# Optimization experiments

Measured on AMD Instinct MI355X. Metric: run time of the kernel, lower is better.

The kernel has to match this reference:

```python
import jax, jax.numpy as jnp
import numpy as np

# Static configuration (matches init_kwargs)
EMBED_DIM = 256
NUM_HEADS = 8
NUM_LEVELS = 4
NUM_POINTS = 16
N_DEGREE = 3
HEAD_DIM = EMBED_DIM // NUM_HEADS
SPATIAL_SHAPES = ((64, 64), (32, 32), (16, 16), (8, 8))  # (H, W) per level
LEN_V = sum(h * w for h, w in SPATIAL_SHAPES)


def _bilinear_gather(v, loc, Hl, Wl):
    """Bilinear sampling with zero padding, align_corners=False.
    v:   [bs, nH, Hl*Wl, hd]  flattened level feature map (per head)
    loc: [bs, nH, Q, 2]       (x, y) in [0, 1]
    returns [bs, nH, Q, hd]
    """
    x = loc[..., 0] * Wl - 0.5
    y = loc[..., 1] * Hl - 0.5
    x0 = jnp.floor(x)
    y0 = jnp.floor(y)
    wx = x - x0
    wy = y - y0
    out = jnp.zeros(v.shape[:2] + (loc.shape[2], v.shape[-1]), v.dtype)
    corners = ((0, 0, (1 - wx) * (1 - wy)), (1, 0, wx * (1 - wy)),
               (0, 1, (1 - wx) * wy), (1, 1, wx * wy))
    for dx, dy, w in corners:
        xi = x0 + dx
        yi = y0 + dy
        valid = (xi >= 0) & (xi < Wl) & (yi >= 0) & (yi < Hl)
        idx = (jnp.clip(yi, 0, Hl - 1) * Wl + jnp.clip(xi, 0, Wl - 1)).astype(jnp.int32)
        g = jnp.take_along_axis(v, idx[..., None], axis=2)  # [bs,nH,Q,hd]
        out = out + g * (w * valid.astype(w.dtype))[..., None]
    return out


def setup_inputs() -> dict:
    key = jax.random.key(0)
    ks = jax.random.split(key, 12)
    bs, Lq = 4, 1024
    s = 0.02
    return {
        "query": jax.random.normal(ks[0], (bs, Lq, EMBED_DIM), jnp.float32),
        # polynomial coefficients for x(l), y(l); scaled so curves stay roughly in [0,1]
        "reference_points": jax.random.uniform(ks[1], (bs, Lq, 2 * (N_DEGREE + 1)), jnp.float32) * 0.25,
        "value": jax.random.normal(ks[2], (bs, LEN_V, EMBED_DIM), jnp.float32),
        "W_value": jax.random.normal(ks[3], (EMBED_DIM, EMBED_DIM), jnp.float32) * s,
        "b_value": jnp.zeros((EMBED_DIM,), jnp.float32),
        "W_offsets": jax.random.normal(ks[4], (EMBED_DIM, NUM_HEADS * NUM_LEVELS * NUM_POINTS * 2), jnp.float32) * s,
        "b_offsets": jax.random.normal(ks[5], (NUM_HEADS * NUM_LEVELS * NUM_POINTS * 2,), jnp.float32) * 0.5,
        "W_attn": jax.random.normal(ks[6], (EMBED_DIM, NUM_HEADS * NUM_LEVELS * NUM_POINTS), jnp.float32) * s,
        "b_attn": jnp.zeros((NUM_HEADS * NUM_LEVELS * NUM_POINTS,), jnp.float32),
        "W_out": jax.random.normal(ks[7], (EMBED_DIM, EMBED_DIM), jnp.float32) * s,
        "b_out": jnp.zeros((EMBED_DIM,), jnp.float32),
    }


def reference(query, reference_points, value, W_value, b_value, W_offsets,
              b_offsets, W_attn, b_attn, W_out, b_out):
    bs, Lq, _ = query.shape
    Lv = value.shape[1]
    nH, nL, nP, hd = NUM_HEADS, NUM_LEVELS, NUM_POINTS, HEAD_DIM

    v = (value @ W_value + b_value).reshape(bs, Lv, nH, hd)

    sampling_offsets = (query @ W_offsets + b_offsets).reshape(bs, Lq, nH, nL, nP, 2)
    attn = jax.nn.softmax((query @ W_attn + b_attn).reshape(bs, Lq, nH, nL * nP), axis=-1)
    attn = attn.reshape(bs, Lq, nH, nL, nP)

    # reference_points last dim == 8: polynomial branch
    lambdaz = jnp.linspace(0.0, 1.0, nP)
    lambdas = jnp.stack([lambdaz ** i for i in range(N_DEGREE, -1, -1)], axis=1)  # [nP, deg+1]
    ref_polys = reference_points.reshape(bs, Lq, 2, N_DEGREE + 1)
    pnts = jnp.einsum('bqcd,pd->bqpc', ref_polys, lambdas)  # [bs,Lq,nP,2] (x,y)

    # offset_normalizer: spatial shapes flipped -> (W, H) per level
    normalizer = jnp.array([[w, h] for (h, w) in SPATIAL_SHAPES], jnp.float32)
    normalizer = normalizer.reshape(1, 1, 1, nL, 1, 2)
    sampling_locations = pnts[:, :, None, None, :, :] + sampling_offsets / normalizer
    # -> [bs, Lq, nH, nL, nP, 2] in [0,1]

    # deformable attention core: per-level bilinear gather + softmax-weighted sum
    out = jnp.zeros((bs, Lq, nH, hd), v.dtype)
    start = 0
    for lvl, (Hl, Wl) in enumerate(SPATIAL_SHAPES):
        v_l = v[:, start:start + Hl * Wl].transpose(0, 2, 1, 3)  # [bs,nH,Hl*Wl,hd]
        loc_l = sampling_locations[:, :, :, lvl]                 # [bs,Lq,nH,nP,2]
        loc_l = loc_l.transpose(0, 2, 1, 3, 4).reshape(bs, nH, Lq * nP, 2)
        sampled = _bilinear_gather(v_l, loc_l, Hl, Wl).reshape(bs, nH, Lq, nP, hd)
        out = out + jnp.einsum('bhqpd,bqhp->bqhd', sampled, attn[:, :, :, lvl])
        start += Hl * Wl

    output = out.reshape(bs, Lq, nH * hd) @ W_out + b_out
    return output, sampling_locations, attn
```

## Files before the change

kernel.cpp:

```cpp
#include <hip/hip_runtime.h>
#include <math.h>

#define BS 4
#define LQ 1024
#define EMB 256
#define NH 8
#define NL 4
#define NP 16
#define HD 32
#define LV 5440
#define LVP 5936
#define KDIM 256

typedef __attribute__((ext_vector_type(8))) short short8;
typedef __attribute__((ext_vector_type(4))) float f32x4;

__device__ inline unsigned short f2bf(float f) {
    unsigned u = __builtin_bit_cast(unsigned, f);
    u += 0x7fff + ((u >> 16) & 1);
    return (unsigned short)(u >> 16);
}



__global__ __launch_bounds__(256) void prep(const float* __restrict__ Wv,
                                            const float* __restrict__ Wo,
                                            const float* __restrict__ Wa,
                                            const float* __restrict__ Wu,
                                            const float* __restrict__ value,
                                            const float* __restrict__ query,
                                            unsigned short* __restrict__ Wt,
                                            unsigned short* __restrict__ val_bf,
                                            unsigned short* __restrict__ qry_bf,
                                            unsigned short* __restrict__ v_pad) {
    const int blk = blockIdx.x;
    const int t = threadIdx.x;
    if (blk < 512) {
        __shared__ float tile[32][33];
        const int n0 = (blk & 63) * 32, k0 = (blk >> 6) * 32;
        const float* src; int N, nloc;
        if (n0 < 256)       { src = Wv; N = 256;  nloc = n0; }
        else if (n0 < 1280) { src = Wo; N = 1024; nloc = n0 - 256; }
        else if (n0 < 1792) { src = Wa; N = 512;  nloc = n0 - 1280; }
        else                { src = Wu; N = 256;  nloc = n0 - 1792; }
        const int tx = t & 31, ty = t >> 5;
#pragma unroll
        for (int i = 0; i < 32; i += 8)
            tile[ty + i][tx] = src[(size_t)(k0 + ty + i) * N + nloc + tx];
        __syncthreads();
        if (t < 128) {
            const int n_loc = t & 31, oct = t >> 5;
            const int n = n0 + n_loc;
            short8 h;
#pragma unroll
            for (int e = 0; e < 8; ++e) h[e] = (short)f2bf(tile[oct * 8 + e][n_loc]);
            const size_t off = ((size_t)(n >> 4) * 8 + (k0 >> 5)) * 512
                             + ((n & 15) + 16 * oct) * 8;
            *(short8*)(Wt + off) = h;
        }
    } else if (blk < 3744) {
        int i; const float* src; unsigned short* dst;
        if (blk < 3232) { i = (blk - 512) * 256 + t;  src = value; dst = val_bf; }
        else            { i = (blk - 3232) * 256 + t; src = query; dst = qry_bf; }
        const int r = i >> 5, oct = i & 31, k0 = oct * 8;
        const float4 f0 = *(const float4*)(src + (size_t)r * KDIM + k0);
        const float4 f1 = *(const float4*)(src + (size_t)r * KDIM + k0 + 4);
        short8 h;
        h[0] = (short)f2bf(f0.x); h[1] = (short)f2bf(f0.y);
        h[2] = (short)f2bf(f0.z); h[3] = (short)f2bf(f0.w);
        h[4] = (short)f2bf(f1.x); h[5] = (short)f2bf(f1.y);
        h[6] = (short)f2bf(f1.z); h[7] = (short)f2bf(f1.w);
        const size_t off = ((size_t)(r >> 4) * 8 + (oct >> 2)) * 512
                         + ((r & 15) + 16 * (oct & 3)) * 8;
        *(short8*)(dst + off) = h;
    } else {
        const int pidx = (blk - 3744) * 8 + (t >> 5);
        const int lane32 = t & 31;
        const unsigned b = (unsigned)pidx / 496u;
        const unsigned rem = (unsigned)pidx - b * 496u;
        int Wd, W2, pb, i;
        if (rem < 260)      { Wd = 64; W2 = 66; pb = 0;    i = rem; }
        else if (rem < 392) { Wd = 32; W2 = 34; pb = 4356; i = rem - 260; }
        else if (rem < 460) { Wd = 16; W2 = 18; pb = 5512; i = rem - 392; }
        else                { Wd = 8;  W2 = 10; pb = 5836; i = rem - 460; }
        int y, x;
        if (i < W2)          { y = 0;      x = i; }
        else if (i < 2 * W2) { y = Wd + 1; x = i - W2; }
        else { const int j = i - 2 * W2; y = 1 + (j >> 1); x = (j & 1) ? (Wd + 1) : 0; }
        const int hh = lane32 >> 2, cq = lane32 & 3;
        const size_t off = (((size_t)(hh * BS + b) * LVP + pb + y * W2 + x) << 5)
                         + cq * 8;
        uint4 z = {0, 0, 0, 0};
        *(uint4*)(v_pad + off) = z;
    }
}

template <int MODE>
__device__ __forceinline__ void gemm_nolds(const unsigned short* __restrict__ A,
                                           const unsigned short* __restrict__ Bt,
                                           const float* __restrict__ bias,
                                           const float* __restrict__ bias2,
                                           const float* __restrict__ refp,
                                           void* __restrict__ Cv,
                                           float* __restrict__ C2,
                                           int N, int bx, int by) {
    const int t = threadIdx.x;
    const int lane = t & 63, w = t >> 6;
    const int quad = lane >> 4, l16 = lane & 15;
    const int wr = w >> 1, wc = w & 1;
    const int row0 = by * 128, col0 = bx * 128;

    const unsigned short* ap = A  + ((size_t)((row0 >> 4) + wr * 4) * 8) * 512 + lane * 8;
    const unsigned short* bp = Bt + ((size_t)((col0 >> 4) + wc * 4) * 8) * 512 + lane * 8;

    f32x4 acc[4][4] = {};

#pragma unroll 2
    for (int kt = 0; kt < 8; ++kt) {
        short8 af[4], bf[4];
#pragma unroll
        for (int mi = 0; mi < 4; ++mi)
            af[mi] = *(const short8*)(ap + (size_t)mi * 4096 + kt * 512);
#pragma unroll
        for (int ni = 0; ni < 4; ++ni)
            bf[ni] = *(const short8*)(bp + (size_t)ni * 4096 + kt * 512);
#pragma unroll
        for (int mi = 0; mi < 4; ++mi)
#pragma unroll
            for (int ni = 0; ni < 4; ++ni)
                acc[mi][ni] = __builtin_amdgcn_mfma_f32_16x16x32_bf16(af[mi], bf[ni],
                                                                      acc[mi][ni], 0, 0, 0);
    }

    if (MODE == 0) {
#pragma unroll
        for (int ni = 0; ni < 4; ++ni) {
            const int c = col0 + wc * 64 + ni * 16 + l16;
            const float bv = bias[c];
#pragma unroll
            for (int mi = 0; mi < 4; ++mi) {
                const int r0 = row0 + wr * 64 + mi * 16 + quad * 4;
#pragma unroll
                for (int rr = 0; rr < 4; ++rr)
                    ((float*)Cv)[(size_t)(r0 + rr) * N + c] = acc[mi][ni][rr] + bv;
            }
        }
    } else if (MODE == 2) {
        unsigned short* C = (unsigned short*)Cv;
        float bv[4];
        int cc[4];
#pragma unroll
        for (int ni = 0; ni < 4; ++ni) {
            cc[ni] = col0 + wc * 64 + ni * 16 + l16;
            bv[ni] = bias[cc[ni]];
        }
#pragma unroll
        for (int mi = 0; mi < 4; ++mi) {
#pragma unroll
            for (int rr = 0; rr < 4; ++rr) {
                const unsigned r = row0 + wr * 64 + mi * 16 + quad * 4 + rr;
                const unsigned b = r / 5440u;
                const unsigned flat = r - b * 5440u;
                unsigned y, x, W2, pb;
                if (flat < 4096)      { y = flat >> 6; x = flat & 63; W2 = 66; pb = 0; }
                else if (flat < 5120) { const unsigned f = flat - 4096; y = f >> 5; x = f & 31; W2 = 34; pb = 4356; }
                else if (flat < 5376) { const unsigned f = flat - 5120; y = f >> 4; x = f & 15; W2 = 18; pb = 5512; }
                else                  { const unsigned f = flat - 5376; y = f >> 3; x = f & 7;  W2 = 10; pb = 5836; }
                const size_t pix = (size_t)(pb + (y + 1) * W2 + (x + 1)) << 5;
#pragma unroll
                for (int ni = 0; ni < 4; ++ni) {
                    const int cc_ = cc[ni];
                    const size_t off = (((size_t)((cc_ >> 5) * BS + b) * LVP) << 5)
                                     + pix + (cc_ & 31);
                    C[off] = f2bf(acc[mi][ni][rr] + bv[ni]);
                }
            }
        }
    } else {
        const bool is_off = (col0 < 1024);
        if (is_off) {
            float* C = (float*)Cv;
#pragma unroll
            for (int ni = 0; ni < 4; ++ni) {
                const int cg = col0 + wc * 64 + ni * 16 + l16;
                const int xy = cg & 1, p = (cg >> 1) & 15, l = (cg >> 5) & 3;
                const float lam = (float)p * (1.0f / 15.0f);
                const float l2 = lam * lam, l3 = l2 * lam;
                const float rW = (l == 0) ? 0.015625f : (l == 1) ? 0.03125f
                                : (l == 2) ? 0.0625f : 0.125f;
                const float bv = bias[cg];
#pragma unroll
                for (int mi = 0; mi < 4; ++mi) {
                    const int r0 = row0 + wr * 64 + mi * 16 + quad * 4;
#pragma unroll
                    for (int rr = 0; rr < 4; ++rr) {
                        const int r = r0 + rr;
                        const float4 rp = *(const float4*)(refp + (size_t)r * 8 + xy * 4);
                        const float poly = rp.x * l3 + rp.y * l2 + rp.z * lam + rp.w;
                        C[(size_t)r * 1024 + cg] = poly + (acc[mi][ni][rr] + bv) * rW;
                    }
                }
            }
        } else {
            const int cabase = col0 - 1024 + wc * 64;
            float bv[4];
#pragma unroll
            for (int ni = 0; ni < 4; ++ni) bv[ni] = bias2[cabase + ni * 16 + l16];
#pragma unroll
            for (int mi = 0; mi < 4; ++mi) {
                const int r0 = row0 + wr * 64 + mi * 16 + quad * 4;
#pragma unroll
                for (int rr = 0; rr < 4; ++rr) {
                    float v0 = acc[mi][0][rr] + bv[0];
                    float v1 = acc[mi][1][rr] + bv[1];
                    float v2 = acc[mi][2][rr] + bv[2];
                    float v3 = acc[mi][3][rr] + bv[3];
                    float mx = fmaxf(fmaxf(v0, v1), fmaxf(v2, v3));
#pragma unroll
                    for (int mk = 1; mk < 16; mk <<= 1) mx = fmaxf(mx, __shfl_xor(mx, mk));
                    v0 = __expf(v0 - mx); v1 = __expf(v1 - mx);
                    v2 = __expf(v2 - mx); v3 = __expf(v3 - mx);
                    float s = v0 + v1 + v2 + v3;
#pragma unroll
                    for (int mk = 1; mk < 16; mk <<= 1) s += __shfl_xor(s, mk);
                    const float inv = 1.0f / s;
                    const size_t rb = (size_t)(r0 + rr) * 512 + cabase + l16;
                    C2[rb]      = v0 * inv;
                    C2[rb + 16] = v1 * inv;
                    C2[rb + 32] = v2 * inv;
                    C2[rb + 48] = v3 * inv;
                }
            }
        }
    }
}

__global__ __launch_bounds__(256, 3) void gemm_fused(const unsigned short* __restrict__ val_bf,
                                                     const unsigned short* __restrict__ qry_bf,
                                                     const unsigned short* __restrict__ Wt,
                                                     const float* __restrict__ b_value,
                                                     const float* __restrict__ b_off,
                                                     const float* __restrict__ b_attn,
                                                     const float* __restrict__ refp,
                                                     unsigned short* __restrict__ v_pad,
                                                     float* __restrict__ loc_out,
                                                     float* __restrict__ attn_out) {
    const int b = blockIdx.x;
    if (b < 340) {
        gemm_nolds<2>(val_bf, Wt, b_value, nullptr, nullptr,
                      v_pad, nullptr, 256, b & 1, b >> 1);
    } else {
        const int b2 = b - 340;
        gemm_nolds<1>(qry_bf, Wt + (size_t)256 * KDIM, b_off, b_attn, refp,
                      loc_out, attn_out, 1536, b2 % 12, b2 / 12);
    }
}

__global__ __launch_bounds__(256, 8) void gemm_outp64(const unsigned short* __restrict__ interm,
                                                      const unsigned short* __restrict__ Wt_out,
                                                      const float* __restrict__ b_out,
                                                      float* __restrict__ out) {
    const int t = threadIdx.x;
    const int lane = t & 63, w = t >> 6;
    const int quad = lane >> 4, l16 = lane & 15;
    const int wr = w >> 1, wc = w & 1;
    const int bx = blockIdx.x & 3, by = blockIdx.x >> 2;
    const int row0 = by * 64 + wr * 32, col0 = bx * 64 + wc * 32;

    const unsigned short* ap = interm + ((size_t)(row0 >> 4) * 8) * 512 + lane * 8;
    const unsigned short* bp = Wt_out + ((size_t)(col0 >> 4) * 8) * 512 + lane * 8;

    f32x4 acc[2][2] = {};

#pragma unroll 2
    for (int kt = 0; kt < 8; ++kt) {
        short8 af[2], bf[2];
#pragma unroll
        for (int mi = 0; mi < 2; ++mi)
            af[mi] = *(const short8*)(ap + (size_t)mi * 4096 + kt * 512);
#pragma unroll
        for (int ni = 0; ni < 2; ++ni)
            bf[ni] = *(const short8*)(bp + (size_t)ni * 4096 + kt * 512);
#pragma unroll
        for (int mi = 0; mi < 2; ++mi)
#pragma unroll
            for (int ni = 0; ni < 2; ++ni)
                acc[mi][ni] = __builtin_amdgcn_mfma_f32_16x16x32_bf16(af[mi], bf[ni],
                                                                      acc[mi][ni], 0, 0, 0);
    }

#pragma unroll
    for (int ni = 0; ni < 2; ++ni) {
        const int c = col0 + ni * 16 + l16;
        const float bv = b_out[c];
#pragma unroll
        for (int mi = 0; mi < 2; ++mi) {
            const int r0 = row0 + mi * 16 + quad * 4;
#pragma unroll
            for (int rr = 0; rr < 4; ++rr)
                out[(size_t)(r0 + rr) * 256 + c] = acc[mi][ni][rr] + bv;
        }
    }
}

__global__ __launch_bounds__(256, 8) void sample_kernel(const unsigned short* __restrict__ v,
                                                        const float* __restrict__ loc,
                                                        const float* __restrict__ attn,
                                                        unsigned short* __restrict__ interm) {
    const int t = threadIdx.x;
    const int h = blockIdx.x & 7;
    const int bq0 = (blockIdx.x >> 3) * 16;

    __shared__ float4 wls[1088];
    __shared__ unsigned short pls[1088];

    {
        const int gloc = t >> 4;
        const int lvl  = (t >> 2) & 3;
        const int pq   = t & 3;
        const int g = (bq0 + gloc) * 8 + h;
        const float4 l01 = *(const float4*)(loc + (size_t)g * 128 + lvl * 32 + pq * 8);
        const float4 l23 = *(const float4*)(loc + (size_t)g * 128 + lvl * 32 + pq * 8 + 4);
        const float4 av  = *(const float4*)(attn + (size_t)g * 64 + lvl * 16 + pq * 4);
        const int Wd = 64 >> lvl;
        const float Wf = (float)Wd;
        const int W2 = Wd + 2;
        const int pb = (lvl == 0) ? 0 : (lvl == 1) ? 4356 : (lvl == 2) ? 5512 : 5836;
        const int ibase = gloc * 64 + lvl * 16 + pq * 4;
        const int pbase = ibase + (ibase >> 4);
        const float lx[4] = {l01.x, l01.z, l23.x, l23.z};
        const float ly[4] = {l01.y, l01.w, l23.y, l23.w};
        const float aw[4] = {av.x, av.y, av.z, av.w};
#pragma unroll
        for (int k = 0; k < 4; ++k) {
            const float x = fmaf(lx[k], Wf, -0.5f);
            const float y = fmaf(ly[k], Wf, -0.5f);
            const float xc = fminf(fmaxf(x, -1.0f), Wf);
            const float yc = fminf(fmaxf(y, -1.0f), Wf);
            const float x0f = fminf(floorf(xc), Wf - 1.0f);
            const float y0f = fminf(floorf(yc), Wf - 1.0f);
            const float wx = xc - x0f, wy = yc - y0f;
            const float iwx = 1.0f - wx, iwy = 1.0f - wy;
            const int px = (int)x0f + 1;
            const int py = (int)y0f + 1;
            const float a = aw[k];
            wls[pbase + k] = make_float4(iwx * iwy * a, wx * iwy * a,
                                         iwx * wy * a,  wx * wy * a);
            pls[pbase + k] = (unsigned short)(pb + py * W2 + px);
        }
    }
    __syncthreads();

    const int bq = bq0 + (t >> 4);
    const int l16i = t & 15;
    const int lvl = l16i >> 2;
    const int cq  = l16i & 3;
    const int b = bq >> 10;
    const int rowoff = ((64 >> lvl) + 2) * 32;

    const unsigned short* vl = v + (((size_t)(h * BS + b) * LVP) << 5) + cq * 8;
    const int wbase = (t >> 4) * 64 + lvl * 16;
    const int wphys = wbase + (wbase >> 4);

    float2 acc2[4] = {};

    auto cvt2 = [](unsigned d) {
        uint2 u; u.x = d << 16; u.y = d & 0xffff0000u;
        return __builtin_bit_cast(float2, u);
    };
    auto cadd = [&](const uint4 q, float wgt) {
        const float2 w2 = make_float2(wgt, wgt);
        acc2[0] += cvt2(q.x) * w2;
        acc2[1] += cvt2(q.y) * w2;
        acc2[2] += cvt2(q.z) * w2;
        acc2[3] += cvt2(q.w) * w2;
    };

#pragma unroll 1
    for (int p = 0; p < 16; ++p) {
        const float4 w = wls[wphys + p];
        const int base = ((int)pls[wphys + p]) << 5;
        const unsigned short* ptr = vl + base;
        const uint4 g00 = *(const uint4*)(ptr);
        const uint4 g10 = *(const uint4*)(ptr + 32);
        const uint4 g01 = *(const uint4*)(ptr + rowoff);
        const uint4 g11 = *(const uint4*)(ptr + rowoff + 32);
        cadd(g00, w.x); cadd(g10, w.y); cadd(g01, w.z); cadd(g11, w.w);
    }

    float a[8] = {acc2[0].x, acc2[0].y, acc2[1].x, acc2[1].y,
                  acc2[2].x, acc2[2].y, acc2[3].x, acc2[3].y};
#pragma unroll
    for (int m = 4; m <= 8; m <<= 1)
#pragma unroll
        for (int k = 0; k < 8; ++k) a[k] += __shfl_xor(a[k], m);

    if (lvl == 0) {
        unsigned short o[8];
#pragma unroll
        for (int k = 0; k < 8; ++k) o[k] = f2bf(a[k]);
        const size_t off = ((size_t)(bq >> 4) * 8 + h) * 512
                         + ((bq & 15) + 16 * cq) * 8;
        *(uint4*)(interm + off) = *(const uint4*)o;
    }
}

extern "C" void kernel_launch(void* const* d_in, const int* in_sizes, int n_in,
                              void* d_out, int out_size, void* d_ws, size_t ws_size,
                              hipStream_t stream) {
    const float* query   = (const float*)d_in[0];
    const float* refp    = (const float*)d_in[1];
    const float* value   = (const float*)d_in[2];
    const float* W_value = (const float*)d_in[3];
    const float* b_value = (const float*)d_in[4];
    const float* W_off   = (const float*)d_in[5];
    const float* b_off   = (const float*)d_in[6];
    const float* W_attn  = (const float*)d_in[7];
    const float* b_attn  = (const float*)d_in[8];
    const float* W_out   = (const float*)d_in[9];
    const float* b_out   = (const float*)d_in[10];

    float* out      = (float*)d_out;
    float* loc_out  = out + 1048576;
    float* attn_out = out + 5242880;

    char* ws = (char*)d_ws;
    unsigned short* v_pad  = (unsigned short*)ws;
    unsigned short* val_bf = (unsigned short*)(ws + 12156928);
    unsigned short* interm = (unsigned short*)(ws + 12156928);
    unsigned short* qry_bf = (unsigned short*)(ws + 23298048);
    unsigned short* Wt_all = (unsigned short*)(ws + 25395200);

    const dim3 blk(256);

    prep<<<3992, blk, 0, stream>>>(W_value, W_off, W_attn, W_out, value, query,
                                   Wt_all, val_bf, qry_bf, v_pad);

    gemm_fused<<<724, blk, 0, stream>>>(val_bf, qry_bf, Wt_all, b_value, b_off,
                                        b_attn, refp, v_pad, loc_out, attn_out);

    sample_kernel<<<(BS * LQ * NH) / 16, blk, 0, stream>>>(v_pad, loc_out, attn_out, interm);

    gemm_outp64<<<256, blk, 0, stream>>>(interm, Wt_all + (size_t)1792 * KDIM, b_out, out);
}
```

Baseline: 149.6 us.

## Fuse projection GEMMs, sampling and output GEMM into one persistent kernel

Replaces the three launches after prep with one persistent kernel of 720 blocks. It loops over the former GEMM, sampling and output-GEMM work items and separates the phases with atomic-counter grid barriers; prep resets the barrier counters. The aim is to remove kernel launch gaps and tail idle time between stages. In exchange, sampling now runs at most about 3 blocks per CU instead of up to 8. The design also depends on all 720 blocks being resident at once, otherwise the spin barriers could deadlock.

```diff
diff --git a/kernel.cpp b/kernel.cpp
--- a/kernel.cpp
+++ b/kernel.cpp
@@ -12,6 +12,8 @@
 #define LVP 5936
 #define KDIM 256
 
+#define TAIL_GRID 720
+
 typedef __attribute__((ext_vector_type(8))) short short8;
 typedef __attribute__((ext_vector_type(4))) float f32x4;
 
@@ -22,6 +24,17 @@
 }
 
 
+__device__ __forceinline__ void gridbar(unsigned* cnt, unsigned n) {
+    __threadfence();
+    __syncthreads();
+    if (threadIdx.x == 0) {
+        __hip_atomic_fetch_add(cnt, 1u, __ATOMIC_ACQ_REL, __HIP_MEMORY_SCOPE_AGENT);
+        while (__hip_atomic_load(cnt, __ATOMIC_RELAXED, __HIP_MEMORY_SCOPE_AGENT) < n)
+            __builtin_amdgcn_s_sleep(16);
+    }
+    __syncthreads();
+    __threadfence();
+}
 
 __global__ __launch_bounds__(256) void prep(const float* __restrict__ Wv,
                                             const float* __restrict__ Wo,
@@ -32,9 +45,11 @@
                                             unsigned short* __restrict__ Wt,
                                             unsigned short* __restrict__ val_bf,
                                             unsigned short* __restrict__ qry_bf,
-                                            unsigned short* __restrict__ v_pad) {
+                                            unsigned short* __restrict__ v_pad,
+                                            unsigned* __restrict__ bar) {
     const int blk = blockIdx.x;
     const int t = threadIdx.x;
+    if (blk == 0 && t == 0) { bar[0] = 0u; bar[1] = 0u; }
     if (blk < 512) {
         __shared__ float tile[32][33];
         const int n0 = (blk & 63) * 32, k0 = (blk >> 6) * 32;
@@ -235,81 +250,13 @@
     }
 }
 
-__global__ __launch_bounds__(256, 3) void gemm_fused(const unsigned short* __restrict__ val_bf,
-                                                     const unsigned short* __restrict__ qry_bf,
-                                                     const unsigned short* __restrict__ Wt,
-                                                     const float* __restrict__ b_value,
-                                                     const float* __restrict__ b_off,
-                                                     const float* __restrict__ b_attn,
-                                                     const float* __restrict__ refp,
-                                                     unsigned short* __restrict__ v_pad,
-                                                     float* __restrict__ loc_out,
-                                                     float* __restrict__ attn_out) {
-    const int b = blockIdx.x;
-    if (b < 340) {
-        gemm_nolds<2>(val_bf, Wt, b_value, nullptr, nullptr,
-                      v_pad, nullptr, 256, b & 1, b >> 1);
-    } else {
-        const int b2 = b - 340;
-        gemm_nolds<1>(qry_bf, Wt + (size_t)256 * KDIM, b_off, b_attn, refp,
-                      loc_out, attn_out, 1536, b2 % 12, b2 / 12);
-    }
-}
-
-__global__ __launch_bounds__(256, 8) void gemm_outp64(const unsigned short* __restrict__ interm,
-                                                      const unsigned short* __restrict__ Wt_out,
-                                                      const float* __restrict__ b_out,
-                                                      float* __restrict__ out) {
-    const int t = threadIdx.x;
-    const int lane = t & 63, w = t >> 6;
-    const int quad = lane >> 4, l16 = lane & 15;
-    const int wr = w >> 1, wc = w & 1;
-    const int bx = blockIdx.x & 3, by = blockIdx.x >> 2;
-    const int row0 = by * 64 + wr * 32, col0 = bx * 64 + wc * 32;
-
-    const unsigned short* ap = interm + ((size_t)(row0 >> 4) * 8) * 512 + lane * 8;
-    const unsigned short* bp = Wt_out + ((size_t)(col0 >> 4) * 8) * 512 + lane * 8;
-
-    f32x4 acc[2][2] = {};
-
-#pragma unroll 2
-    for (int kt = 0; kt < 8; ++kt) {
-        short8 af[2], bf[2];
-#pragma unroll
-        for (int mi = 0; mi < 2; ++mi)
-            af[mi] = *(const short8*)(ap + (size_t)mi * 4096 + kt * 512);
-#pragma unroll
-        for (int ni = 0; ni < 2; ++ni)
-            bf[ni] = *(const short8*)(bp + (size_t)ni * 4096 + kt * 512);
-#pragma unroll
-        for (int mi = 0; mi < 2; ++mi)
-#pragma unroll
-            for (int ni = 0; ni < 2; ++ni)
-                acc[mi][ni] = __builtin_amdgcn_mfma_f32_16x16x32_bf16(af[mi], bf[ni],
-                                                                      acc[mi][ni], 0, 0, 0);
-    }
-
-#pragma unroll
-    for (int ni = 0; ni < 2; ++ni) {
-        const int c = col0 + ni * 16 + l16;
-        const float bv = b_out[c];
-#pragma unroll
-        for (int mi = 0; mi < 2; ++mi) {
-            const int r0 = row0 + mi * 16 + quad * 4;
-#pragma unroll
-            for (int rr = 0; rr < 4; ++rr)
-                out[(size_t)(r0 + rr) * 256 + c] = acc[mi][ni][rr] + bv;
-        }
-    }
-}
-
-__global__ __launch_bounds__(256, 8) void sample_kernel(const unsigned short* __restrict__ v,
-                                                        const float* __restrict__ loc,
-                                                        const float* __restrict__ attn,
-                                                        unsigned short* __restrict__ interm) {
-    const int t = threadIdx.x;
-    const int h = blockIdx.x & 7;
-    const int bq0 = (blockIdx.x >> 3) * 16;
+__device__ __forceinline__ void sample_chunk(int sbid, int t,
+                                             const unsigned short* __restrict__ v,
+                                             const float* __restrict__ loc,
+                                             const float* __restrict__ attn,
+                                             unsigned short* __restrict__ interm) {
+    const int h = sbid & 7;
+    const int bq0 = (sbid >> 3) * 16;
 
     __shared__ float4 wls[1088];
     __shared__ unsigned short pls[1088];
@@ -405,6 +352,89 @@
     }
 }
 
+__global__ __launch_bounds__(256, 3) void fused_tail(const unsigned short* __restrict__ val_bf,
+                                                     const unsigned short* __restrict__ qry_bf,
+                                                     const unsigned short* __restrict__ Wt,
+                                                     const float* __restrict__ b_value,
+                                                     const float* __restrict__ b_off,
+                                                     const float* __restrict__ b_attn,
+                                                     const float* __restrict__ refp,
+                                                     unsigned short* __restrict__ v_pad,
+                                                     float* __restrict__ loc_out,
+                                                     float* __restrict__ attn_out,
+                                                     unsigned short* __restrict__ interm,
+                                                     const unsigned short* __restrict__ Wt_out,
+                                                     const float* __restrict__ b_out,
+                                                     float* __restrict__ out,
+                                                     unsigned* __restrict__ bar) {
+    const int t = threadIdx.x;
+
+#pragma unroll 1
+    for (int g = blockIdx.x; g < 724; g += TAIL_GRID) {
+        if (g < 340) {
+            gemm_nolds<2>(val_bf, Wt, b_value, nullptr, nullptr,
+                          v_pad, nullptr, 256, g & 1, g >> 1);
+        } else {
+            const int g2 = g - 340;
+            gemm_nolds<1>(qry_bf, Wt + (size_t)256 * KDIM, b_off, b_attn, refp,
+                          loc_out, attn_out, 1536, g2 % 12, g2 / 12);
+        }
+    }
+
+    gridbar(bar, TAIL_GRID);
+
+#pragma unroll 1
+    for (int sb = blockIdx.x; sb < 2048; sb += TAIL_GRID) {
+        sample_chunk(sb, t, v_pad, loc_out, attn_out, interm);
+        __syncthreads();
+    }
+
+    gridbar(bar + 1, TAIL_GRID);
+
+    if (blockIdx.x < 256) {
+        const int lane = t & 63, w = t >> 6;
+        const int quad = lane >> 4, l16 = lane & 15;
+        const int wr = w >> 1, wc = w & 1;
+        const int bx = blockIdx.x & 3, by = blockIdx.x >> 2;
+        const int row0 = by * 64 + wr * 32, col0 = bx * 64 + wc * 32;
+
+        const unsigned short* ap = interm + ((size_t)(row0 >> 4) * 8) * 512 + lane * 8;
+        const unsigned short* bp = Wt_out + ((size_t)(col0 >> 4) * 8) * 512 + lane * 8;
+
+        f32x4 acc[2][2] = {};
+
+#pragma unroll 2
+        for (int kt = 0; kt < 8; ++kt) {
+            short8 af[2], bf[2];
+#pragma unroll
+            for (int mi = 0; mi < 2; ++mi)
+                af[mi] = *(const short8*)(ap + (size_t)mi * 4096 + kt * 512);
+#pragma unroll
+            for (int ni = 0; ni < 2; ++ni)
+                bf[ni] = *(const short8*)(bp + (size_t)ni * 4096 + kt * 512);
+#pragma unroll
+            for (int mi = 0; mi < 2; ++mi)
+#pragma unroll
+                for (int ni = 0; ni < 2; ++ni)
+                    acc[mi][ni] = __builtin_amdgcn_mfma_f32_16x16x32_bf16(af[mi], bf[ni],
+                                                                          acc[mi][ni], 0, 0, 0);
+        }
+
+#pragma unroll
+        for (int ni = 0; ni < 2; ++ni) {
+            const int c = col0 + ni * 16 + l16;
+            const float bv = b_out[c];
+#pragma unroll
+            for (int mi = 0; mi < 2; ++mi) {
+                const int r0 = row0 + mi * 16 + quad * 4;
+#pragma unroll
+                for (int rr = 0; rr < 4; ++rr)
+                    out[(size_t)(r0 + rr) * 256 + c] = acc[mi][ni][rr] + bv;
+            }
+        }
+    }
+}
+
 extern "C" void kernel_launch(void* const* d_in, const int* in_sizes, int n_in,
                               void* d_out, int out_size, void* d_ws, size_t ws_size,
                               hipStream_t stream) {
@@ -430,16 +460,16 @@
     unsigned short* interm = (unsigned short*)(ws + 12156928);
     unsigned short* qry_bf = (unsigned short*)(ws + 23298048);
     unsigned short* Wt_all = (unsigned short*)(ws + 25395200);
+    unsigned*       bar    = (unsigned*)(ws + 26443776);
+    const unsigned short* Wt_outp = Wt_all + (size_t)1792 * KDIM;
 
     const dim3 blk(256);
 
     prep<<<3992, blk, 0, stream>>>(W_value, W_off, W_attn, W_out, value, query,
-                                   Wt_all, val_bf, qry_bf, v_pad);
-
-    gemm_fused<<<724, blk, 0, stream>>>(val_bf, qry_bf, Wt_all, b_value, b_off,
-                                        b_attn, refp, v_pad, loc_out, attn_out);
-
-    sample_kernel<<<(BS * LQ * NH) / 16, blk, 0, stream>>>(v_pad, loc_out, attn_out, interm);
-
-    gemm_outp64<<<256, blk, 0, stream>>>(interm, Wt_all + (size_t)1792 * KDIM, b_out, out);
-}
+                                   Wt_all, val_bf, qry_bf, v_pad, bar);
+
+    fused_tail<<<TAIL_GRID, blk, 0, stream>>>(val_bf, qry_bf, Wt_all, b_value,
+                                              b_off, b_attn, refp, v_pad,
+                                              loc_out, attn_out, interm,
+                                              Wt_outp, b_out, out, bar);
+}
```

After: 540.7 us. 3.61x slower.
